# Optimization experiments

Hardware: AMD Instinct MI355X
Metric: run time of the kernel (lower is better)

Reference implementation:

```python
import jax, jax.numpy as jnp
import numpy as np

# snntorch default surrogate: ATan with alpha=2.0
@jax.custom_vjp
def spike_fn(x):
    return (x > 0).astype(x.dtype)

def _spike_fwd(x):
    return spike_fn(x), x

def _spike_bwd(x, g):
    alpha = 2.0
    return (g * (alpha / 2.0) / (1.0 + (jnp.pi / 2.0 * alpha * x) ** 2),)

spike_fn.defvjp(_spike_fwd, _spike_bwd)

B, T, D_IN, H, OUT = 256, 25, 768, 2048, 10

def setup_inputs() -> dict:
    key = jax.random.key(0)
    ks = jax.random.split(key, 5)
    def lin(k, fan_in, fan_out):
        bound = 1.0 / np.sqrt(fan_in)
        kw, kb = jax.random.split(k)
        W = jax.random.uniform(kw, (fan_out, fan_in), minval=-bound, maxval=bound, dtype=jnp.float32)
        b = jax.random.uniform(kb, (fan_out,), minval=-bound, maxval=bound, dtype=jnp.float32)
        return W, b
    W1, b1 = lin(ks[0], D_IN, H)
    W2, b2 = lin(ks[1], H, H)
    W3, b3 = lin(ks[2], H, H)
    W4, b4 = lin(ks[3], H, OUT)
    x = jax.random.normal(ks[4], (B, T, D_IN), dtype=jnp.float32)
    beta = jnp.asarray(0.9, jnp.float32)
    thr = jnp.asarray(1.0, jnp.float32)
    return dict(x=x, W1=W1, b1=b1, W2=W2, b2=b2, W3=W3, b3=b3, W4=W4, b4=b4,
                beta1=beta, beta2=beta, beta3=beta, beta4=beta,
                thr1=thr, thr2=thr, thr3=thr, thr4=thr)

def reference(x, W1, b1, W2, b2, W3, b3, W4, b4,
              beta1, beta2, beta3, beta4, thr1, thr2, thr3, thr4):
    # snntorch Leaky (reset_mechanism='subtract', learn_beta, learn_threshold):
    #   reset = detach(heaviside(mem_prev - thr))
    #   mem   = clip(beta,0,1)*mem_prev + cur - reset*thr
    #   spk   = heaviside(mem - thr)   (ATan surrogate in bwd)
    def lif(cur, mem, beta, thr):
        b = jnp.clip(beta, 0.0, 1.0)
        reset = jax.lax.stop_gradient(spike_fn(mem - thr))
        mem = b * mem + cur - reset * thr
        spk = spike_fn(mem - thr)
        return spk, mem

    Bx = x.shape[0]
    def step(carry, x_t):
        m1, m2, m3, m4 = carry
        c1 = x_t @ W1.T + b1; s1, m1 = lif(c1, m1, beta1, thr1)
        c2 = s1 @ W2.T + b2; s2, m2 = lif(c2, m2, beta2, thr2)
        c3 = s2 @ W3.T + b3; s3, m3 = lif(c3, m3, beta3, thr3)
        c4 = s3 @ W4.T + b4; s4, m4 = lif(c4, m4, beta4, thr4)
        return (m1, m2, m3, m4), (s1, s2, s3, s4, m1, m2, m3, m4, c1, c2, c3, c4)

    init = (jnp.zeros((Bx, W1.shape[0]), x.dtype),
            jnp.zeros((Bx, W2.shape[0]), x.dtype),
            jnp.zeros((Bx, W3.shape[0]), x.dtype),
            jnp.zeros((Bx, W4.shape[0]), x.dtype))
    _, recs = jax.lax.scan(step, init, jnp.swapaxes(x, 0, 1))  # time-major scan
    # recs = (spk1..4, mem1..4, cur1..4), each stacked [T, B, feat]
    return recs
```

## Files before the change

### kernel.cpp

```cpp
#include <hip/hip_runtime.h>


typedef int v4i  __attribute__((ext_vector_type(4)));
typedef int v16i __attribute__((ext_vector_type(16)));

#define T_   25
#define BB   256
#define DIN  768
#define HH   2048
#define PT   (BB*HH)
#define PT4  (BB*10)

__global__ __launch_bounds__(256)
void k_decomp_x(const float* __restrict__ x, char* __restrict__ xpl)
{
    int gid = blockIdx.x * 256 + threadIdx.x;
    int r = gid / 48, rem = gid % 48;
    int kc = rem >> 1, h = rem & 1;
    int t = r >> 8, b = r & 255;
    const float* src = x + ((size_t)b * T_ + t) * DIN + kc * 32 + h * 16;
    alignas(16) char dig[4][16];
#pragma unroll
    for (int e = 0; e < 16; ++e) {
        long long V = llround((double)src[e] * 268435456.0);
#pragma unroll
        for (int p = 0; p < 3; ++p) {
            int d = (int)(V & 255); if (d >= 128) d -= 256;
            dig[p][e] = (char)d; V = (V - d) >> 8;
        }
        dig[3][e] = (char)V;
    }
    size_t base = (((size_t)(r >> 5) * 24 + kc) * 4) * 1024 + (size_t)(h * 32 + (r & 31)) * 16;
#pragma unroll
    for (int p = 0; p < 4; ++p)
        *(int4*)(xpl + base + (size_t)p * 1024) = *(const int4*)dig[p];
}

template<int NDIG, int QSH, int KC>
__global__ __launch_bounds__(256)
void k_decomp_w(const float* __restrict__ W, char* __restrict__ wpl, int K)
{
    int gid = blockIdx.x * 256 + threadIdx.x;
    int n = gid / (KC * 2), rem = gid % (KC * 2);
    int kc = rem >> 1, h = rem & 1;
    const float* src = W + (size_t)n * K + kc * 32 + h * 16;
    const double scale = (double)(1ULL << QSH);
    alignas(16) char dig[NDIG][16];
#pragma unroll
    for (int e = 0; e < 16; ++e) {
        long long V = llround((double)src[e] * scale);
#pragma unroll
        for (int p = 0; p < NDIG - 1; ++p) {
            int d = (int)(V & 255); if (d >= 128) d -= 256;
            dig[p][e] = (char)d; V = (V - d) >> 8;
        }
        dig[NDIG - 1][e] = (char)V;
    }
    size_t base = (((size_t)(n >> 5) * KC + kc) * NDIG) * 1024 + (size_t)(h * 32 + (n & 31)) * 16;
#pragma unroll
    for (int p = 0; p < NDIG; ++p)
        *(int4*)(wpl + base + (size_t)p * 1024) = *(const int4*)dig[p];
}

__global__ __launch_bounds__(256)
void k_gemm1(const char* __restrict__ xpl, const char* __restrict__ wpl,
             const float* __restrict__ bias, float* __restrict__ c_out,
             float* __restrict__ res_out)
{
    int wid = threadIdx.x >> 6, l = threadIdx.x & 63;
    int nt = blockIdx.x;
    int mt = blockIdx.y * 4 + wid;
    v16i acc[5] = {};
    const char* ab = xpl + ((size_t)mt * 24) * 4 * 1024 + (size_t)l * 16;
    const char* wb = wpl + ((size_t)nt * 24) * 4 * 1024 + (size_t)l * 16;
#pragma unroll 2
    for (int kc = 0; kc < 24; ++kc) {
        v4i xv[4], wv[4];
#pragma unroll
        for (int p = 0; p < 4; ++p) {
            xv[p] = *(const v4i*)(ab + (size_t)(kc * 4 + p) * 1024);
            wv[p] = *(const v4i*)(wb + (size_t)(kc * 4 + p) * 1024);
        }
        acc[4] = __builtin_amdgcn_mfma_i32_32x32x32_i8(xv[3], wv[3], acc[4], 0,0,0);
        acc[3] = __builtin_amdgcn_mfma_i32_32x32x32_i8(xv[2], wv[3], acc[3], 0,0,0);
        acc[3] = __builtin_amdgcn_mfma_i32_32x32x32_i8(xv[3], wv[2], acc[3], 0,0,0);
        acc[2] = __builtin_amdgcn_mfma_i32_32x32x32_i8(xv[1], wv[3], acc[2], 0,0,0);
        acc[2] = __builtin_amdgcn_mfma_i32_32x32x32_i8(xv[2], wv[2], acc[2], 0,0,0);
        acc[2] = __builtin_amdgcn_mfma_i32_32x32x32_i8(xv[3], wv[1], acc[2], 0,0,0);
        acc[1] = __builtin_amdgcn_mfma_i32_32x32x32_i8(xv[0], wv[3], acc[1], 0,0,0);
        acc[1] = __builtin_amdgcn_mfma_i32_32x32x32_i8(xv[1], wv[2], acc[1], 0,0,0);
        acc[1] = __builtin_amdgcn_mfma_i32_32x32x32_i8(xv[2], wv[1], acc[1], 0,0,0);
        acc[1] = __builtin_amdgcn_mfma_i32_32x32x32_i8(xv[3], wv[0], acc[1], 0,0,0);
        acc[0] = __builtin_amdgcn_mfma_i32_32x32x32_i8(xv[0], wv[2], acc[0], 0,0,0);
        acc[0] = __builtin_amdgcn_mfma_i32_32x32x32_i8(xv[1], wv[1], acc[0], 0,0,0);
        acc[0] = __builtin_amdgcn_mfma_i32_32x32x32_i8(xv[2], wv[0], acc[0], 0,0,0);
    }
    int half = l >> 5, lr = l & 31;
    int col = nt * 32 + lr;
    double bv = (double)bias[col];
#pragma unroll
    for (int e = 0; e < 16; ++e) {
        int row = (e & 3) + 8 * (e >> 2) + 4 * half;
        int r = mt * 32 + row;
        double hv = (((((double)acc[4][e] * 256.0 + (double)acc[3][e]) * 256.0
                      + (double)acc[2][e]) * 256.0 + (double)acc[1][e]) * 256.0 + (double)acc[0][e]);
        double v = hv * 7.105427357601002e-15 + bv;
        float cf = (float)v;
        float rf = (float)(v - (double)cf);
        size_t off = (size_t)r * HH + col;
        c_out[off] = cf; res_out[off] = rf;
    }
}

__global__ __launch_bounds__(256)
void k_gemm23(const char* __restrict__ aq, const char* __restrict__ wpl,
              const float* __restrict__ bias,
              float* __restrict__ c_out, float* __restrict__ res_out)
{
    int wid = threadIdx.x >> 6, l = threadIdx.x & 63;
    int half = l >> 5, lr = l & 31;
    int nt = blockIdx.x;
    int mt = blockIdx.y * 4 + wid;
    v16i acc[4] = {};
    const char* ab = aq + (size_t)mt * 65536 + (size_t)l * 16;
    const char* wb = wpl + ((size_t)nt * 64) * 4 * 1024 + (size_t)l * 16;
#pragma unroll 4
    for (int kc = 0; kc < 64; ++kc) {
        v4i a  = *(const v4i*)(ab + (size_t)kc * 1024);
        v4i w0 = *(const v4i*)(wb + (size_t)(kc * 4 + 0) * 1024);
        v4i w1 = *(const v4i*)(wb + (size_t)(kc * 4 + 1) * 1024);
        v4i w2 = *(const v4i*)(wb + (size_t)(kc * 4 + 2) * 1024);
        v4i w3 = *(const v4i*)(wb + (size_t)(kc * 4 + 3) * 1024);
        acc[0] = __builtin_amdgcn_mfma_i32_32x32x32_i8(a, w0, acc[0], 0,0,0);
        acc[1] = __builtin_amdgcn_mfma_i32_32x32x32_i8(a, w1, acc[1], 0,0,0);
        acc[2] = __builtin_amdgcn_mfma_i32_32x32x32_i8(a, w2, acc[2], 0,0,0);
        acc[3] = __builtin_amdgcn_mfma_i32_32x32x32_i8(a, w3, acc[3], 0,0,0);
    }
    int col = nt * 32 + lr;
    double bv = (double)bias[col];
#pragma unroll
    for (int e = 0; e < 16; ++e) {
        int row = (e & 3) + 8 * (e >> 2) + 4 * half;
        size_t off = (size_t)(mt * 32 + row) * HH + col;
        double dot = ((((double)acc[3][e] * 256.0 + (double)acc[2][e]) * 256.0
                      + (double)acc[1][e]) * 256.0 + (double)acc[0][e]) * 2.9103830456733704e-11;
        double v = dot + bv;
        float cf = (float)v;
        float rf = (float)(v - (double)cf);
        c_out[off] = cf; res_out[off] = rf;
    }
}

template<bool SWZ>
__global__ __launch_bounds__(256)
void k_scan(const float* __restrict__ c, float* __restrict__ res_m,
            float* __restrict__ s, char* __restrict__ sq,
            const float* __restrict__ beta_p, const float* __restrict__ thr_p)
{
    int idx = blockIdx.x * 256 + threadIdx.x;
    int b = idx >> 11, n = idx & 2047;
    double beta = fmin(fmax((double)*beta_p, 0.0), 1.0);
    double thr  = (double)*thr_p;
    double mem = 0.0;
    for (int t = 0; t < T_; ++t) {
        size_t off = (size_t)t * PT + idx;
        double cur = (double)c[off] + (double)res_m[off];
        double reset = (mem > thr) ? 1.0 : 0.0;
        mem = beta * mem + cur - reset * thr;
        bool sp = mem > thr;
        res_m[off] = (float)mem;
        s[off] = sp ? 1.f : 0.f;
        if (SWZ) {
            int r = t * 256 + b;
            size_t sa = ((size_t)((r >> 5) * 64 + (n >> 5))) * 1024
                      + (size_t)((((n >> 4) & 1) * 32 + (r & 31))) * 16 + (n & 15);
            sq[sa] = sp ? 1 : 0;
        }
    }
}

__global__ __launch_bounds__(256)
void k_gemm4(const float* __restrict__ A, const float* __restrict__ W,
             const float* __restrict__ bias,
             float* __restrict__ c_out, float* __restrict__ res_out)
{
    int wid = threadIdx.x >> 6, lane = threadIdx.x & 63;
    int i = blockIdx.x * 4 + wid;
    double a[32];
#pragma unroll
    for (int m = 0; m < 32; ++m)
        a[m] = (double)A[(size_t)i * HH + lane + 64 * m];
    for (int j = 0; j < 10; ++j) {
        double s = 0.0;
#pragma unroll
        for (int m = 0; m < 32; ++m)
            s += a[m] * (double)W[(size_t)j * HH + lane + 64 * m];
#pragma unroll
        for (int o = 32; o > 0; o >>= 1)
            s += __shfl_down(s, o);
        if (lane == 0) {
            double v = s + (double)bias[j];
            float cf = (float)v;
            float rf = (float)(v - (double)cf);
            c_out[i * 10 + j] = cf; res_out[i * 10 + j] = rf;
        }
    }
}

__global__ __launch_bounds__(256)
void k_scan4(const float* __restrict__ c, float* __restrict__ res_m,
             float* __restrict__ s,
             const float* __restrict__ beta_p, const float* __restrict__ thr_p)
{
    int idx = blockIdx.x * 256 + threadIdx.x;
    if (idx >= PT4) return;
    double beta = fmin(fmax((double)*beta_p, 0.0), 1.0);
    double thr  = (double)*thr_p;
    double mem = 0.0;
    for (int t = 0; t < T_; ++t) {
        size_t off = (size_t)t * PT4 + idx;
        double cur = (double)c[off] + (double)res_m[off];
        double reset = (mem > thr) ? 1.0 : 0.0;
        mem = beta * mem + cur - reset * thr;
        res_m[off] = (float)mem;
        s[off] = (mem > thr) ? 1.f : 0.f;
    }
}

#define BM 32
#define BN 64
#define BK 32
__global__ __launch_bounds__(256)
void gemm_lif_f64(const float* __restrict__ A, int lda, const float* __restrict__ W,
                  const float* __restrict__ bias, const double* __restrict__ m64_in,
                  const float* __restrict__ m32_in, double* __restrict__ m64_out,
                  float* __restrict__ cur_out, float* __restrict__ mem_out, float* __restrict__ spk_out,
                  const float* __restrict__ beta_p, const float* __restrict__ thr_p, int K, int N)
{
    __shared__ double As[BK][BM + 4];
    __shared__ double Ws[BK][BN + 4];
    const int tid = threadIdx.x;
    const int bm = blockIdx.y * BM, bn = blockIdx.x * BN;
    const int tx = tid & 15, ty = tid >> 4;
    const int n0 = tx * 4, m0 = ty * 2;
    const int arow = tid >> 3, acol = (tid & 7) * 4;
    double acc[2][4] = {{0,0,0,0},{0,0,0,0}};
    for (int kt = 0; kt < K; kt += BK) {
        float4 av = *reinterpret_cast<const float4*>(A + (size_t)(bm + arow) * lda + kt + acol);
        As[acol+0][arow]=av.x; As[acol+1][arow]=av.y; As[acol+2][arow]=av.z; As[acol+3][arow]=av.w;
#pragma unroll
        for (int r = 0; r < 2; ++r) {
            int n = arow + r * 32;
            float4 wv = *reinterpret_cast<const float4*>(W + (size_t)(bn + n) * K + kt + acol);
            Ws[acol+0][n]=wv.x; Ws[acol+1][n]=wv.y; Ws[acol+2][n]=wv.z; Ws[acol+3][n]=wv.w;
        }
        __syncthreads();
#pragma unroll
        for (int k = 0; k < BK; ++k) {
            double2 a  = *reinterpret_cast<const double2*>(&As[k][m0]);
            double2 w0 = *reinterpret_cast<const double2*>(&Ws[k][n0]);
            double2 w1 = *reinterpret_cast<const double2*>(&Ws[k][n0 + 2]);
            acc[0][0]+=a.x*w0.x; acc[0][1]+=a.x*w0.y; acc[0][2]+=a.x*w1.x; acc[0][3]+=a.x*w1.y;
            acc[1][0]+=a.y*w0.x; acc[1][1]+=a.y*w0.y; acc[1][2]+=a.y*w1.x; acc[1][3]+=a.y*w1.y;
        }
        __syncthreads();
    }
    const double beta = fmin(fmax((double)*beta_p, 0.0), 1.0);
    const double thr  = (double)*thr_p;
#pragma unroll
    for (int r = 0; r < 2; ++r) {
        const size_t off = (size_t)(bm + m0 + r) * N + bn + n0;
        float4 cf, mf, sf;
        float* cfp=&cf.x; float* mfp=&mf.x; float* sfp=&sf.x;
#pragma unroll
        for (int j = 0; j < 4; ++j) {
            double cur = acc[r][j] + (double)bias[bn + n0 + j];
            double mp = m64_in ? m64_in[off + j] : (m32_in ? (double)m32_in[off + j] : 0.0);
            double reset = (mp > thr) ? 1.0 : 0.0;
            double mem = beta * mp + cur - reset * thr;
            cfp[j]=(float)cur; mfp[j]=(float)mem; sfp[j]=(mem > thr)?1.f:0.f;
            if (m64_out) m64_out[off + j] = mem;
        }
        *reinterpret_cast<float4*>(cur_out + off) = cf;
        *reinterpret_cast<float4*>(mem_out + off) = mf;
        *reinterpret_cast<float4*>(spk_out + off) = sf;
    }
}

__global__ __launch_bounds__(256)
void k_fc4_lif(const float* __restrict__ A, const float* __restrict__ W,
               const float* __restrict__ bias, double* __restrict__ m4ws,
               float* __restrict__ c4, float* __restrict__ m4, float* __restrict__ s4,
               const float* __restrict__ beta_p, const float* __restrict__ thr_p, int t0)
{
    int wid = threadIdx.x >> 6, lane = threadIdx.x & 63;
    int i = blockIdx.x * 4 + wid;
    double a[32];
#pragma unroll
    for (int m = 0; m < 32; ++m)
        a[m] = (double)A[(size_t)i * HH + lane + 64 * m];
    double beta = fmin(fmax((double)*beta_p, 0.0), 1.0);
    double thr  = (double)*thr_p;
    for (int j = 0; j < 10; ++j) {
        double s = 0.0;
#pragma unroll
        for (int m = 0; m < 32; ++m)
            s += a[m] * (double)W[(size_t)j * HH + lane + 64 * m];
#pragma unroll
        for (int o = 32; o > 0; o >>= 1)
            s += __shfl_down(s, o);
        if (lane == 0) {
            double cur = s + (double)bias[j];
            double mp = t0 ? 0.0 : m4ws[i * 10 + j];
            double reset = (mp > thr) ? 1.0 : 0.0;
            double mem = beta * mp + cur - reset * thr;
            c4[i * 10 + j] = (float)cur; m4[i * 10 + j] = (float)mem;
            s4[i * 10 + j] = (mem > thr) ? 1.f : 0.f;
            m4ws[i * 10 + j] = mem;
        }
    }
}

extern "C" void kernel_launch(void* const* d_in, const int* in_sizes, int n_in,
                              void* d_out, int out_size, void* d_ws, size_t ws_size,
                              hipStream_t stream) {
    const float* x  = (const float*)d_in[0];
    const float* W1 = (const float*)d_in[1];  const float* b1 = (const float*)d_in[2];
    const float* W2 = (const float*)d_in[3];  const float* b2 = (const float*)d_in[4];
    const float* W3 = (const float*)d_in[5];  const float* b3 = (const float*)d_in[6];
    const float* W4 = (const float*)d_in[7];  const float* b4 = (const float*)d_in[8];
    const float* beta1 = (const float*)d_in[9];  const float* beta2 = (const float*)d_in[10];
    const float* beta3 = (const float*)d_in[11]; const float* beta4 = (const float*)d_in[12];
    const float* thr1 = (const float*)d_in[13];  const float* thr2 = (const float*)d_in[14];
    const float* thr3 = (const float*)d_in[15];  const float* thr4 = (const float*)d_in[16];

    float* out = (float*)d_out;
    const size_t SB = (size_t)T_ * PT, SB4 = (size_t)T_ * PT4;
    float* s1 = out;            float* s2 = out + SB;   float* s3 = out + 2*SB; float* s4 = out + 3*SB;
    float* m1 = s4 + SB4;       float* m2 = m1 + SB;    float* m3 = m1 + 2*SB;  float* m4 = m1 + 3*SB;
    float* c1 = m4 + SB4;       float* c2 = c1 + SB;    float* c3 = c1 + 2*SB;  float* c4 = c1 + 3*SB;

    const size_t XPL = 4ull*6400*768;
    const size_t W1PL = 4ull*2048*768;
    const size_t W23PL = 4ull*2048*2048;
    const size_t SQ = 6400ull*2048;
    size_t need = XPL + W1PL + 2*W23PL + 2*SQ;

    if (ws_size >= need) {
        char* w = (char*)d_ws;
        char* xpl  = w;              char* w1pl = xpl + XPL;
        char* w2pl = w1pl + W1PL;    char* w3pl = w2pl + W23PL;
        char* s1q  = w3pl + W23PL;   char* s2q  = s1q + SQ;

        k_decomp_x<<<1200, 256, 0, stream>>>(x, xpl);
        k_decomp_w<4,35,24><<<384, 256, 0, stream>>>(W1, w1pl, 768);
        k_decomp_w<4,35,64><<<1024, 256, 0, stream>>>(W2, w2pl, 2048);
        k_decomp_w<4,35,64><<<1024, 256, 0, stream>>>(W3, w3pl, 2048);

        k_gemm1<<<dim3(64, 50), 256, 0, stream>>>(xpl, w1pl, b1, c1, m1);
        k_scan<true><<<2048, 256, 0, stream>>>(c1, m1, s1, s1q, beta1, thr1);
        k_gemm23<<<dim3(64, 50), 256, 0, stream>>>(s1q, w2pl, b2, c2, m2);
        k_scan<true><<<2048, 256, 0, stream>>>(c2, m2, s2, s2q, beta2, thr2);
        k_gemm23<<<dim3(64, 50), 256, 0, stream>>>(s2q, w3pl, b3, c3, m3);
        k_scan<false><<<2048, 256, 0, stream>>>(c3, m3, s3, nullptr, beta3, thr3);
        k_gemm4<<<1600, 256, 0, stream>>>(s3, W4, b4, c4, m4);
        k_scan4<<<10, 256, 0, stream>>>(c4, m4, s4, beta4, thr4);
        return;
    }

    const size_t NL = PT;
    const size_t WS_NEED = (3 * NL + PT4) * sizeof(double);
    const bool use64 = (d_ws != nullptr) && (ws_size >= WS_NEED);
    double* wsd = (double*)d_ws;
    double* mm1 = use64 ? wsd : nullptr;
    double* mm2 = use64 ? wsd + NL : nullptr;
    double* mm3 = use64 ? wsd + 2 * NL : nullptr;
    double* mm4 = use64 ? wsd + 3 * NL : nullptr;
    const dim3 grid(HH / BN, BB / BM);
    for (int t = 0; t < T_; ++t) {
        size_t po = (size_t)t * PT, po4 = (size_t)t * PT4;
        gemm_lif_f64<<<grid, 256, 0, stream>>>(x + (size_t)t * DIN, T_ * DIN, W1, b1,
            t ? mm1 : nullptr, t ? m1 + po - PT : nullptr, mm1,
            c1 + po, m1 + po, s1 + po, beta1, thr1, DIN, HH);
        gemm_lif_f64<<<grid, 256, 0, stream>>>(s1 + po, HH, W2, b2,
            t ? mm2 : nullptr, t ? m2 + po - PT : nullptr, mm2,
            c2 + po, m2 + po, s2 + po, beta2, thr2, HH, HH);
        gemm_lif_f64<<<grid, 256, 0, stream>>>(s2 + po, HH, W3, b3,
            t ? mm3 : nullptr, t ? m3 + po - PT : nullptr, mm3,
            c3 + po, m3 + po, s3 + po, beta3, thr3, HH, HH);
        k_fc4_lif<<<64, 256, 0, stream>>>(s3 + po, W4, b4,
            mm4 ? mm4 : (double*)d_ws, c4 + po4, m4 + po4, s4 + po4, beta4, thr4, t == 0);
    }
}
```

Before: 707.2 us.

## Stage weight planes in LDS and share across eight M-tile waves

The int8 MFMA GEMM kernels for layers 1-3 now use 512-thread blocks with eight waves, each owning one 32-row M tile. They cooperatively copy 8 K-chunks of weight digit planes into 32KB of shared memory, then read weights from LDS instead of each wave fetching them from global memory. This halves the number of blocks and cuts redundant global and L2 weight traffic. In exchange it adds two barriers per K block with no double buffering, so the load and compute phases are serialized, and the larger blocks may reduce occupancy.

```diff
diff --git a/kernel.cpp b/kernel.cpp
--- a/kernel.cpp
+++ b/kernel.cpp
@@ -62,38 +62,52 @@
         *(int4*)(wpl + base + (size_t)p * 1024) = *(const int4*)dig[p];
 }
 
-__global__ __launch_bounds__(256)
+__global__ __launch_bounds__(512)
 void k_gemm1(const char* __restrict__ xpl, const char* __restrict__ wpl,
              const float* __restrict__ bias, float* __restrict__ c_out,
              float* __restrict__ res_out)
 {
-    int wid = threadIdx.x >> 6, l = threadIdx.x & 63;
+    __shared__ char wlds[32768];
+    int tid = threadIdx.x;
+    int wm = tid >> 6, l = tid & 63;
     int nt = blockIdx.x;
-    int mt = blockIdx.y * 4 + wid;
+    int mt = blockIdx.y * 8 + wm;
     v16i acc[5] = {};
     const char* ab = xpl + ((size_t)mt * 24) * 4 * 1024 + (size_t)l * 16;
-    const char* wb = wpl + ((size_t)nt * 24) * 4 * 1024 + (size_t)l * 16;
-#pragma unroll 2
-    for (int kc = 0; kc < 24; ++kc) {
-        v4i xv[4], wv[4];
-#pragma unroll
-        for (int p = 0; p < 4; ++p) {
-            xv[p] = *(const v4i*)(ab + (size_t)(kc * 4 + p) * 1024);
-            wv[p] = *(const v4i*)(wb + (size_t)(kc * 4 + p) * 1024);
-        }
-        acc[4] = __builtin_amdgcn_mfma_i32_32x32x32_i8(xv[3], wv[3], acc[4], 0,0,0);
-        acc[3] = __builtin_amdgcn_mfma_i32_32x32x32_i8(xv[2], wv[3], acc[3], 0,0,0);
-        acc[3] = __builtin_amdgcn_mfma_i32_32x32x32_i8(xv[3], wv[2], acc[3], 0,0,0);
-        acc[2] = __builtin_amdgcn_mfma_i32_32x32x32_i8(xv[1], wv[3], acc[2], 0,0,0);
-        acc[2] = __builtin_amdgcn_mfma_i32_32x32x32_i8(xv[2], wv[2], acc[2], 0,0,0);
-        acc[2] = __builtin_amdgcn_mfma_i32_32x32x32_i8(xv[3], wv[1], acc[2], 0,0,0);
-        acc[1] = __builtin_amdgcn_mfma_i32_32x32x32_i8(xv[0], wv[3], acc[1], 0,0,0);
-        acc[1] = __builtin_amdgcn_mfma_i32_32x32x32_i8(xv[1], wv[2], acc[1], 0,0,0);
-        acc[1] = __builtin_amdgcn_mfma_i32_32x32x32_i8(xv[2], wv[1], acc[1], 0,0,0);
-        acc[1] = __builtin_amdgcn_mfma_i32_32x32x32_i8(xv[3], wv[0], acc[1], 0,0,0);
-        acc[0] = __builtin_amdgcn_mfma_i32_32x32x32_i8(xv[0], wv[2], acc[0], 0,0,0);
-        acc[0] = __builtin_amdgcn_mfma_i32_32x32x32_i8(xv[1], wv[1], acc[0], 0,0,0);
-        acc[0] = __builtin_amdgcn_mfma_i32_32x32x32_i8(xv[2], wv[0], acc[0], 0,0,0);
+
+    for (int kcb = 0; kcb < 3; ++kcb) {
+        __syncthreads();
+        const char* src = wpl + ((size_t)(nt * 24 + kcb * 8)) * 4 * 1024;
+#pragma unroll
+        for (int i = 0; i < 4; ++i) {
+            int off = tid * 16 + i * 8192;
+            *(int4*)(wlds + off) = *(const int4*)(src + off);
+        }
+        __syncthreads();
+#pragma unroll
+        for (int kc = 0; kc < 8; ++kc) {
+            const char* a8 = ab + (size_t)(kcb * 8 + kc) * 4096;
+            const char* w8 = wlds + (size_t)kc * 4096 + (size_t)l * 16;
+            v4i xv[4], wv[4];
+#pragma unroll
+            for (int p = 0; p < 4; ++p) {
+                xv[p] = *(const v4i*)(a8 + (size_t)p * 1024);
+                wv[p] = *(const v4i*)(w8 + (size_t)p * 1024);
+            }
+            acc[4] = __builtin_amdgcn_mfma_i32_32x32x32_i8(xv[3], wv[3], acc[4], 0,0,0);
+            acc[3] = __builtin_amdgcn_mfma_i32_32x32x32_i8(xv[2], wv[3], acc[3], 0,0,0);
+            acc[3] = __builtin_amdgcn_mfma_i32_32x32x32_i8(xv[3], wv[2], acc[3], 0,0,0);
+            acc[2] = __builtin_amdgcn_mfma_i32_32x32x32_i8(xv[1], wv[3], acc[2], 0,0,0);
+            acc[2] = __builtin_amdgcn_mfma_i32_32x32x32_i8(xv[2], wv[2], acc[2], 0,0,0);
+            acc[2] = __builtin_amdgcn_mfma_i32_32x32x32_i8(xv[3], wv[1], acc[2], 0,0,0);
+            acc[1] = __builtin_amdgcn_mfma_i32_32x32x32_i8(xv[0], wv[3], acc[1], 0,0,0);
+            acc[1] = __builtin_amdgcn_mfma_i32_32x32x32_i8(xv[1], wv[2], acc[1], 0,0,0);
+            acc[1] = __builtin_amdgcn_mfma_i32_32x32x32_i8(xv[2], wv[1], acc[1], 0,0,0);
+            acc[1] = __builtin_amdgcn_mfma_i32_32x32x32_i8(xv[3], wv[0], acc[1], 0,0,0);
+            acc[0] = __builtin_amdgcn_mfma_i32_32x32x32_i8(xv[0], wv[2], acc[0], 0,0,0);
+            acc[0] = __builtin_amdgcn_mfma_i32_32x32x32_i8(xv[1], wv[1], acc[0], 0,0,0);
+            acc[0] = __builtin_amdgcn_mfma_i32_32x32x32_i8(xv[2], wv[0], acc[0], 0,0,0);
+        }
     }
     int half = l >> 5, lr = l & 31;
     int col = nt * 32 + lr;
@@ -112,29 +126,42 @@
     }
 }
 
-__global__ __launch_bounds__(256)
+__global__ __launch_bounds__(512)
 void k_gemm23(const char* __restrict__ aq, const char* __restrict__ wpl,
               const float* __restrict__ bias,
               float* __restrict__ c_out, float* __restrict__ res_out)
 {
-    int wid = threadIdx.x >> 6, l = threadIdx.x & 63;
+    __shared__ char wlds[32768];
+    int tid = threadIdx.x;
+    int wm = tid >> 6, l = tid & 63;
     int half = l >> 5, lr = l & 31;
     int nt = blockIdx.x;
-    int mt = blockIdx.y * 4 + wid;
+    int mt = blockIdx.y * 8 + wm;
     v16i acc[4] = {};
     const char* ab = aq + (size_t)mt * 65536 + (size_t)l * 16;
-    const char* wb = wpl + ((size_t)nt * 64) * 4 * 1024 + (size_t)l * 16;
-#pragma unroll 4
-    for (int kc = 0; kc < 64; ++kc) {
-        v4i a  = *(const v4i*)(ab + (size_t)kc * 1024);
-        v4i w0 = *(const v4i*)(wb + (size_t)(kc * 4 + 0) * 1024);
-        v4i w1 = *(const v4i*)(wb + (size_t)(kc * 4 + 1) * 1024);
-        v4i w2 = *(const v4i*)(wb + (size_t)(kc * 4 + 2) * 1024);
-        v4i w3 = *(const v4i*)(wb + (size_t)(kc * 4 + 3) * 1024);
-        acc[0] = __builtin_amdgcn_mfma_i32_32x32x32_i8(a, w0, acc[0], 0,0,0);
-        acc[1] = __builtin_amdgcn_mfma_i32_32x32x32_i8(a, w1, acc[1], 0,0,0);
-        acc[2] = __builtin_amdgcn_mfma_i32_32x32x32_i8(a, w2, acc[2], 0,0,0);
-        acc[3] = __builtin_amdgcn_mfma_i32_32x32x32_i8(a, w3, acc[3], 0,0,0);
+
+    for (int kcb = 0; kcb < 8; ++kcb) {
+        __syncthreads();
+        const char* src = wpl + ((size_t)(nt * 64 + kcb * 8)) * 4 * 1024;
+#pragma unroll
+        for (int i = 0; i < 4; ++i) {
+            int off = tid * 16 + i * 8192;
+            *(int4*)(wlds + off) = *(const int4*)(src + off);
+        }
+        __syncthreads();
+#pragma unroll
+        for (int kc = 0; kc < 8; ++kc) {
+            v4i a  = *(const v4i*)(ab + (size_t)(kcb * 8 + kc) * 1024);
+            const char* w8 = wlds + (size_t)kc * 4096 + (size_t)l * 16;
+            v4i w0 = *(const v4i*)(w8);
+            v4i w1 = *(const v4i*)(w8 + 1024);
+            v4i w2 = *(const v4i*)(w8 + 2048);
+            v4i w3 = *(const v4i*)(w8 + 3072);
+            acc[0] = __builtin_amdgcn_mfma_i32_32x32x32_i8(a, w0, acc[0], 0,0,0);
+            acc[1] = __builtin_amdgcn_mfma_i32_32x32x32_i8(a, w1, acc[1], 0,0,0);
+            acc[2] = __builtin_amdgcn_mfma_i32_32x32x32_i8(a, w2, acc[2], 0,0,0);
+            acc[3] = __builtin_amdgcn_mfma_i32_32x32x32_i8(a, w3, acc[3], 0,0,0);
+        }
     }
     int col = nt * 32 + lr;
     double bv = (double)bias[col];
@@ -357,11 +384,11 @@
         k_decomp_w<4,35,64><<<1024, 256, 0, stream>>>(W2, w2pl, 2048);
         k_decomp_w<4,35,64><<<1024, 256, 0, stream>>>(W3, w3pl, 2048);
 
-        k_gemm1<<<dim3(64, 50), 256, 0, stream>>>(xpl, w1pl, b1, c1, m1);
+        k_gemm1<<<dim3(64, 25), 512, 0, stream>>>(xpl, w1pl, b1, c1, m1);
         k_scan<true><<<2048, 256, 0, stream>>>(c1, m1, s1, s1q, beta1, thr1);
-        k_gemm23<<<dim3(64, 50), 256, 0, stream>>>(s1q, w2pl, b2, c2, m2);
+        k_gemm23<<<dim3(64, 25), 512, 0, stream>>>(s1q, w2pl, b2, c2, m2);
         k_scan<true><<<2048, 256, 0, stream>>>(c2, m2, s2, s2q, beta2, thr2);
-        k_gemm23<<<dim3(64, 50), 256, 0, stream>>>(s2q, w3pl, b3, c3, m3);
+        k_gemm23<<<dim3(64, 25), 512, 0, stream>>>(s2q, w3pl, b3, c3, m3);
         k_scan<false><<<2048, 256, 0, stream>>>(c3, m3, s3, nullptr, beta3, thr3);
         k_gemm4<<<1600, 256, 0, stream>>>(s3, W4, b4, c4, m4);
         k_scan4<<<10, 256, 0, stream>>>(c4, m4, s4, beta4, thr4);
```

New measurement: 587.9 us. 16.9% less time.
